# Kernel optimization log

Measured on AMD Instinct MI355X. Metric: run time of the kernel, lower is better.

Reference implementation:

```python
import jax, jax.numpy as jnp
import numpy as np

H_GRU = 32  # GRU hidden size fixed to 32 in the module


def setup_inputs() -> dict:
    key = jax.random.key(0)
    ks = jax.random.split(key, 12)
    B, C_in, H, W = 64, 64, 48, 160
    C_out = 64
    s_in = 1.0 / np.sqrt(C_in)
    s_h = 1.0 / np.sqrt(H_GRU)
    u = lambda k, shape: jax.random.uniform(k, shape, jnp.float32, -s_h, s_h)
    return {
        "x": jax.random.normal(ks[0], (B, C_in, H, W), jnp.float32),
        "conv_w": jax.random.normal(ks[1], (C_out, C_in), jnp.float32) * s_in,
        "conv_b": jax.random.normal(ks[2], (C_out,), jnp.float32) * s_in,
        "wih_f": u(ks[3], (3 * H_GRU, C_out)),
        "whh_f": u(ks[4], (3 * H_GRU, H_GRU)),
        "bih_f": u(ks[5], (3 * H_GRU,)),
        "bhh_f": u(ks[6], (3 * H_GRU,)),
        "wih_b": u(ks[7], (3 * H_GRU, C_out)),
        "whh_b": u(ks[8], (3 * H_GRU, H_GRU)),
        "bih_b": u(ks[9], (3 * H_GRU,)),
        "bhh_b": u(ks[10], (3 * H_GRU,)),
    }


def _gru_scan(pre, whh, bhh):
    # pre: [N, T, 3H] input-side gate pre-activations (already x@Wih^T + bih)
    N = pre.shape[0]

    def step(h, g):
        gh = h @ whh.T + bhh
        gi_r, gi_z, gi_n = jnp.split(g, 3, axis=-1)
        gh_r, gh_z, gh_n = jnp.split(gh, 3, axis=-1)
        r = jax.nn.sigmoid(gi_r + gh_r)
        z = jax.nn.sigmoid(gi_z + gh_z)
        n = jnp.tanh(gi_n + r * gh_n)
        h_new = (1.0 - z) * n + z * h
        return h_new, h_new

    h0 = jnp.zeros((N, H_GRU), pre.dtype)
    _, ys = jax.lax.scan(step, h0, jnp.swapaxes(pre, 0, 1))  # ys: [T, N, H]
    return jnp.swapaxes(ys, 0, 1)  # [N, T, H]


def reference(x, conv_w, conv_b, wih_f, whh_f, bih_f, bhh_f,
              wih_b, whh_b, bih_b, bhh_b):
    B, C_in, H, W = x.shape
    # 1x1 conv fused with the NCHW->NHWC permute
    y = jnp.einsum('bchw,oc->bhwo', x, conv_w) + conv_b  # [B, H, W, C_out]
    C_out = y.shape[-1]
    seq = y.reshape(B * H, W, C_out)  # GRU batch = B*H, seq_len = W
    # forward direction
    pre_f = jnp.einsum('ntc,gc->ntg', seq, wih_f) + bih_f
    out_f = _gru_scan(pre_f, whh_f, bhh_f)
    # backward direction: scan reversed sequence, then flip output back
    seq_r = seq[:, ::-1, :]
    pre_b = jnp.einsum('ntc,gc->ntg', seq_r, wih_b) + bih_b
    out_b = _gru_scan(pre_b, whh_b, bhh_b)[:, ::-1, :]
    out = jnp.concatenate([out_f, out_b], axis=-1)  # [B*H, W, 2*H_GRU]
    out = out.reshape(B, H, W, 2 * H_GRU)
    return jnp.transpose(out, (0, 3, 1, 2))  # back to NCHW
```

## Files before the change

### kernel.cpp

```cpp
#include <hip/hip_runtime.h>


typedef _Float16 f16x8 __attribute__((ext_vector_type(8)));
typedef _Float16 f16x4 __attribute__((ext_vector_type(4)));
typedef __fp16   pk16  __attribute__((ext_vector_type(2)));
typedef float    f32x4 __attribute__((ext_vector_type(4)));

#define HWSTRIDE 7680
#define WS_WHH2_OFF 24576
#define WS_BIAS_OFF 36864
#define WS_X16_OFF  65536
#define NWIN 20

__global__ void fold_weights(const float* __restrict__ conv_w,
                             const float* __restrict__ conv_b,
                             const float* __restrict__ wih_f,
                             const float* __restrict__ bih_f,
                             const float* __restrict__ bhh_f,
                             const float* __restrict__ wih_b,
                             const float* __restrict__ bih_b,
                             const float* __restrict__ bhh_b,
                             const float* __restrict__ whh_f,
                             const float* __restrict__ whh_b,
                             void* wsv)
{
    _Float16* W2   = (_Float16*)wsv;
    _Float16* whh2 = (_Float16*)((char*)wsv + WS_WHH2_OFF);
    float*    bias = (float*)((char*)wsv + WS_BIAS_OFF);
    const int idx = blockIdx.x * 256 + threadIdx.x;
    if (idx < 12288) {
        const int d = idx / 6144, r = idx % 6144, g = r / 64, c = r % 64;
        const float* wih = d ? wih_b : wih_f;
        float acc = 0.f;
        for (int o = 0; o < 64; ++o) acc += wih[g * 64 + o] * conv_w[o * 64 + c];
        W2[idx] = (_Float16)acc;
    } else if (idx < 18432) {
        const int e2 = idx - 12288;
        const int dd = e2 / 3072, rr = e2 % 3072, g = rr / 32, k = rr % 32;
        const int qq = k >> 3, ee = k & 7;
        const int jsrc = (ee < 4) ? (qq * 4 + ee) : (16 + qq * 4 + (ee - 4));
        const float* whh = dd ? whh_b : whh_f;
        whh2[e2] = (_Float16)whh[g * 32 + jsrc];
    } else if (idx < 18688) {
        const int e = idx - 18432;
        const int d = e >> 7, rr = e & 127, kind = rr >> 5, j = rr & 31;
        const float* wih = d ? wih_b : wih_f;
        const float* bih = d ? bih_b : bih_f;
        const float* bhh = d ? bhh_b : bhh_f;
        float v;
        if (kind == 0 || kind == 1) {
            const int g = j + kind * 32;
            float b2 = bih[g];
            for (int o = 0; o < 64; ++o) b2 += wih[g * 64 + o] * conv_b[o];
            v = b2 + bhh[g];
        } else if (kind == 2) {
            const int g = j + 64;
            float b2 = bih[g];
            for (int o = 0; o < 64; ++o) b2 += wih[g * 64 + o] * conv_b[o];
            v = b2;
        } else {
            v = bhh[j + 64];
        }
        bias[(d * 4 + kind) * 32 + j] = v;
    }
}

static __device__ __forceinline__ unsigned pkh(float a, float b) {
    pk16 p = __builtin_amdgcn_cvt_pkrtz(a, b);
    return __builtin_bit_cast(unsigned, p);
}

__global__ __launch_bounds__(256, 2)
void xpose(const float* __restrict__ x, _Float16* __restrict__ x16)
{
    __shared__ _Float16 tile[16 * 16 * 64];
    const int bid = blockIdx.x;
    const int wc  = bid % 10;
    const int hg  = (bid / 10) % 3;
    const int b   = bid / 30;
    const int t   = threadIdx.x;
    const int s   = t >> 4;
    const int c2  = t & 15;
    const float* xb = x + (size_t)b * 64 * HWSTRIDE + (size_t)(hg * 16) * 160 + wc * 16;

    float4 pf[4][4];
    #pragma unroll
    for (int cc = 0; cc < 4; ++cc)
        #pragma unroll
        for (int k = 0; k < 4; ++k)
            pf[cc][k] = *(const float4*)(xb + (size_t)(c2 * 4 + cc) * HWSTRIDE
                                         + (size_t)s * 160 + k * 4);
    #pragma unroll
    for (int k = 0; k < 4; ++k)
        #pragma unroll
        for (int m = 0; m < 4; ++m) {
            const int w = k * 4 + m;
            uint2 v;
            v.x = pkh(((const float*)&pf[0][k])[m], ((const float*)&pf[1][k])[m]);
            v.y = pkh(((const float*)&pf[2][k])[m], ((const float*)&pf[3][k])[m]);
            const int baddr = (s * 2048 + w * 128 + c2 * 8) ^ ((s & 7) << 4);
            *(uint2*)((char*)tile + baddr) = v;
        }
    __syncthreads();
    #pragma unroll
    for (int k = 0; k < 4; ++k) {
        const int w  = k * 4 + (t >> 6);
        const int ss = (t & 63) >> 2;
        const int c0 = (t & 3) * 16;
        uint2 dv[4];
        #pragma unroll
        for (int j = 0; j < 4; ++j) {
            const int baddr = (ss * 2048 + w * 128 + c0 * 2 + j * 8) ^ ((ss & 7) << 4);
            dv[j] = *(const uint2*)((char*)tile + baddr);
        }
        _Float16* op = x16 + ((size_t)(b * 3 + hg) * 160 + wc * 16 + w) * 1024 + ss * 64 + c0;
        *(uint4*)(op)     = make_uint4(dv[0].x, dv[0].y, dv[1].x, dv[1].y);
        *(uint4*)(op + 8) = make_uint4(dv[2].x, dv[2].y, dv[3].x, dv[3].y);
    }
}

__global__ __launch_bounds__(64, 1)
void gru_fused9(const _Float16* __restrict__ x16,
                const void* __restrict__ wsv,
                float* __restrict__ out)
{
    const int bid   = blockIdx.x;
    const int d     = bid & 1;
    const int slice = bid >> 1;
    const int b     = slice / 3;
    const int hg    = slice % 3;
    const int h0    = hg * 16;
    const int lane  = threadIdx.x;
    const int q     = lane >> 4;
    const int s16   = lane & 15;

    const _Float16* W2 = (const _Float16*)wsv + (size_t)d * 96 * 64;
    f16x8 W2A[6][2];
    #pragma unroll
    for (int gt = 0; gt < 6; ++gt)
        #pragma unroll
        for (int kt = 0; kt < 2; ++kt)
            W2A[gt][kt] = *(const f16x8*)&W2[(gt * 16 + s16) * 64 + kt * 32 + q * 8];
    const _Float16* whh2 = (const _Float16*)((const char*)wsv + WS_WHH2_OFF)
                           + (size_t)d * 96 * 32;
    f16x8 whhA[6];
    #pragma unroll
    for (int gt = 0; gt < 6; ++gt)
        whhA[gt] = *(const f16x8*)&whh2[(gt * 16 + s16) * 32 + q * 8];
    const float* bias = (const float*)((const char*)wsv + WS_BIAS_OFF) + d * 128;
    float biasC[6][4];
    #pragma unroll
    for (int gt = 0; gt < 6; ++gt)
        #pragma unroll
        for (int r = 0; r < 4; ++r)
            biasC[gt][r] = bias[(gt >> 1) * 32 + (gt & 1) * 16 + 4 * q + r];
    float bhN[2][4];
    #pragma unroll
    for (int jh = 0; jh < 2; ++jh)
        #pragma unroll
        for (int r = 0; r < 4; ++r)
            bhN[jh][r] = bias[96 + jh * 16 + 4 * q + r];

    const _Float16* xsl = x16 + (size_t)slice * 160 * 1024 + s16 * 64 + q * 8;
    float* ob = out + ((size_t)b * 64 + d * 32) * HWSTRIDE + (size_t)(h0 + s16) * 160;

    f16x8 B0r[4], B1r[4];
    auto loadB = [&](int s, f16x8& B0d, f16x8& B1d) {
        const _Float16* p = xsl + (size_t)(d ? (159 - s) : s) * 1024;
        B0d = *(const f16x8*)(p);
        B1d = *(const f16x8*)(p + 32);
    };
    #pragma unroll
    for (int s0 = 0; s0 < 4; ++s0) loadB(s0, B0r[s0], B1r[s0]);

    f16x8 hB = {};
    f16x8 hB8[8];
    float hprev[8];
    #pragma unroll
    for (int uu = 0; uu < 8; ++uu) hprev[uu] = 0.f;

    #pragma unroll 1
    for (int i = 0; i < NWIN; ++i) {
        #pragma unroll
        for (int tt = 0; tt < 8; ++tt) {
            const int s = i * 8 + tt;
            f32x4 aR0 = {biasC[0][0], biasC[0][1], biasC[0][2], biasC[0][3]};
            f32x4 aR1 = {biasC[1][0], biasC[1][1], biasC[1][2], biasC[1][3]};
            f32x4 aZ0 = {biasC[2][0], biasC[2][1], biasC[2][2], biasC[2][3]};
            f32x4 aZ1 = {biasC[3][0], biasC[3][1], biasC[3][2], biasC[3][3]};
            f32x4 pN0 = {biasC[4][0], biasC[4][1], biasC[4][2], biasC[4][3]};
            f32x4 pN1 = {biasC[5][0], biasC[5][1], biasC[5][2], biasC[5][3]};
            f32x4 hN0 = {bhN[0][0], bhN[0][1], bhN[0][2], bhN[0][3]};
            f32x4 hN1 = {bhN[1][0], bhN[1][1], bhN[1][2], bhN[1][3]};
            aR0 = __builtin_amdgcn_mfma_f32_16x16x32_f16(W2A[0][0], B0r[tt & 3], aR0, 0, 0, 0);
            aR0 = __builtin_amdgcn_mfma_f32_16x16x32_f16(W2A[0][1], B1r[tt & 3], aR0, 0, 0, 0);
            aR1 = __builtin_amdgcn_mfma_f32_16x16x32_f16(W2A[1][0], B0r[tt & 3], aR1, 0, 0, 0);
            aR1 = __builtin_amdgcn_mfma_f32_16x16x32_f16(W2A[1][1], B1r[tt & 3], aR1, 0, 0, 0);
            aZ0 = __builtin_amdgcn_mfma_f32_16x16x32_f16(W2A[2][0], B0r[tt & 3], aZ0, 0, 0, 0);
            aZ0 = __builtin_amdgcn_mfma_f32_16x16x32_f16(W2A[2][1], B1r[tt & 3], aZ0, 0, 0, 0);
            aZ1 = __builtin_amdgcn_mfma_f32_16x16x32_f16(W2A[3][0], B0r[tt & 3], aZ1, 0, 0, 0);
            aZ1 = __builtin_amdgcn_mfma_f32_16x16x32_f16(W2A[3][1], B1r[tt & 3], aZ1, 0, 0, 0);
            pN0 = __builtin_amdgcn_mfma_f32_16x16x32_f16(W2A[4][0], B0r[tt & 3], pN0, 0, 0, 0);
            pN0 = __builtin_amdgcn_mfma_f32_16x16x32_f16(W2A[4][1], B1r[tt & 3], pN0, 0, 0, 0);
            pN1 = __builtin_amdgcn_mfma_f32_16x16x32_f16(W2A[5][0], B0r[tt & 3], pN1, 0, 0, 0);
            pN1 = __builtin_amdgcn_mfma_f32_16x16x32_f16(W2A[5][1], B1r[tt & 3], pN1, 0, 0, 0);
            aR0 = __builtin_amdgcn_mfma_f32_16x16x32_f16(whhA[0], hB, aR0, 0, 0, 0);
            aR1 = __builtin_amdgcn_mfma_f32_16x16x32_f16(whhA[1], hB, aR1, 0, 0, 0);
            aZ0 = __builtin_amdgcn_mfma_f32_16x16x32_f16(whhA[2], hB, aZ0, 0, 0, 0);
            aZ1 = __builtin_amdgcn_mfma_f32_16x16x32_f16(whhA[3], hB, aZ1, 0, 0, 0);
            hN0 = __builtin_amdgcn_mfma_f32_16x16x32_f16(whhA[4], hB, hN0, 0, 0, 0);
            hN1 = __builtin_amdgcn_mfma_f32_16x16x32_f16(whhA[5], hB, hN1, 0, 0, 0);
            if (tt < 4) {
                loadB(s + 4, B0r[tt & 3], B1r[tt & 3]);
            } else if (i + 1 < NWIN) {
                loadB(s + 4, B0r[tt & 3], B1r[tt & 3]);
            }
            float hn[8];
            #pragma unroll
            for (int r = 0; r < 4; ++r) {
                const float rr = __builtin_amdgcn_rcpf(1.f + __expf(-aR0[r]));
                const float zz = __builtin_amdgcn_rcpf(1.f + __expf(-aZ0[r]));
                float ta = fmaf(rr, hN0[r], pN0[r]);
                ta = fminf(fmaxf(ta, -15.f), 15.f);
                const float e2 = __expf(2.f * ta);
                const float nn = (e2 - 1.f) * __builtin_amdgcn_rcpf(e2 + 1.f);
                hn[r] = (1.f - zz) * nn + zz * hprev[r];
            }
            #pragma unroll
            for (int r = 0; r < 4; ++r) {
                const float rr = __builtin_amdgcn_rcpf(1.f + __expf(-aR1[r]));
                const float zz = __builtin_amdgcn_rcpf(1.f + __expf(-aZ1[r]));
                float ta = fmaf(rr, hN1[r], pN1[r]);
                ta = fminf(fmaxf(ta, -15.f), 15.f);
                const float e2 = __expf(2.f * ta);
                const float nn = (e2 - 1.f) * __builtin_amdgcn_rcpf(e2 + 1.f);
                hn[4 + r] = (1.f - zz) * nn + zz * hprev[4 + r];
            }
            {
                uint4 hu;
                hu.x = pkh(hn[0], hn[1]); hu.y = pkh(hn[2], hn[3]);
                hu.z = pkh(hn[4], hn[5]); hu.w = pkh(hn[6], hn[7]);
                hB = __builtin_bit_cast(f16x8, hu);
            }
            hB8[tt] = hB;
            #pragma unroll
            for (int uu = 0; uu < 8; ++uu) hprev[uu] = hn[uu];
        }
        {
            const int w0 = d ? (152 - 8 * i) : (8 * i);
            #pragma unroll
            for (int e = 0; e < 8; ++e) {
                const int j = (e >> 2) * 16 + 4 * q + (e & 3);
                float* pw = ob + (size_t)j * HWSTRIDE + w0;
                if (d == 0) {
                    *(float4*)(pw)     = make_float4((float)hB8[0][e], (float)hB8[1][e],
                                                     (float)hB8[2][e], (float)hB8[3][e]);
                    *(float4*)(pw + 4) = make_float4((float)hB8[4][e], (float)hB8[5][e],
                                                     (float)hB8[6][e], (float)hB8[7][e]);
                } else {
                    *(float4*)(pw)     = make_float4((float)hB8[7][e], (float)hB8[6][e],
                                                     (float)hB8[5][e], (float)hB8[4][e]);
                    *(float4*)(pw + 4) = make_float4((float)hB8[3][e], (float)hB8[2][e],
                                                     (float)hB8[1][e], (float)hB8[0][e]);
                }
            }
        }
    }
}

#define BAR() do { asm volatile("s_waitcnt lgkmcnt(0)" ::: "memory"); \
                   __builtin_amdgcn_s_barrier();                      \
                   asm volatile("" ::: "memory"); } while (0)

__global__ __launch_bounds__(128, 1)
void gru_fused8(const float* __restrict__ x,
                const void* __restrict__ wsv,
                float* __restrict__ out)
{
    __shared__ __align__(16) _Float16 xt[1024 * 8];
    __shared__ __align__(16) _Float16 spre[2 * 8 * 16 * 96];

    const int bid  = blockIdx.x;
    const int d    = bid / 192;
    const int g    = bid % 192;
    const int b    = g / 3;
    const int h0   = (g % 3) * 16;
    const int lane = threadIdx.x & 63;
    const int wave = threadIdx.x >> 6;
    const int sw   = bid & 1;
    const int q    = lane >> 4;
    const int s16  = lane & 15;

    const float* xb = x + (size_t)b * 64 * HWSTRIDE + (size_t)h0 * 160;

    if (wave != sw) {
        const _Float16* W2 = (const _Float16*)wsv + (size_t)d * 96 * 64;
        f16x8 W2A[6][2];
        #pragma unroll
        for (int gt = 0; gt < 6; ++gt)
            #pragma unroll
            for (int kt = 0; kt < 2; ++kt)
                W2A[gt][kt] = *(const f16x8*)&W2[(gt * 16 + s16) * 64 + kt * 32 + q * 8];
        const float* bias = (const float*)((const char*)wsv + WS_BIAS_OFF) + d * 128;
        float biasC[6][4];
        #pragma unroll
        for (int gt = 0; gt < 6; ++gt)
            #pragma unroll
            for (int r = 0; r < 4; ++r)
                biasC[gt][r] = bias[(gt >> 1) * 32 + (gt & 1) * 16 + 4 * q + r];

        float4 pf[32];
        auto load_win = [&](int wi) {
            const int w0 = d ? (152 - 8 * wi) : (8 * wi);
            #pragma unroll
            for (int k = 0; k < 16; ++k) {
                const int row = lane + 64 * k;
                const float* p = xb + (size_t)(row >> 4) * HWSTRIDE + (row & 15) * 160 + w0;
                pf[2 * k]     = *(const float4*)p;
                pf[2 * k + 1] = *(const float4*)(p + 4);
            }
        };
        auto write_xt = [&]() {
            #pragma unroll
            for (int k = 0; k < 16; ++k) {
                const int row = lane + 64 * k;
                uint4 v;
                v.x = pkh(pf[2*k].x,   pf[2*k].y);
                v.y = pkh(pf[2*k].z,   pf[2*k].w);
                v.z = pkh(pf[2*k+1].x, pf[2*k+1].y);
                v.w = pkh(pf[2*k+1].z, pf[2*k+1].w);
                *(uint4*)&xt[row * 8] = v;
            }
        };
        auto project = [&](int wi) {
            _Float16* sp = &spre[(wi & 1) * 12288];
            for (int tt = 0; tt < 8; ++tt) {
                const int wl = d ? (7 - tt) : tt;
                const int base0 = (q * 8) * 128 + s16 * 8 + wl;
                f16x8 B0, B1;
                #pragma unroll
                for (int e = 0; e < 8; ++e) {
                    B0[e] = xt[base0 + e * 128];
                    B1[e] = xt[base0 + e * 128 + 4096];
                }
                #pragma unroll
                for (int gt = 0; gt < 6; ++gt) {
                    f32x4 acc = {biasC[gt][0], biasC[gt][1], biasC[gt][2], biasC[gt][3]};
                    acc = __builtin_amdgcn_mfma_f32_16x16x32_f16(W2A[gt][0], B0, acc, 0, 0, 0);
                    acc = __builtin_amdgcn_mfma_f32_16x16x32_f16(W2A[gt][1], B1, acc, 0, 0, 0);
                    uint2 v; v.x = pkh(acc[0], acc[1]); v.y = pkh(acc[2], acc[3]);
                    const int col = (gt * 16 + 4 * q) ^ ((s16 & 7) << 2);
                    *(uint2*)&sp[(tt * 16 + s16) * 96 + col] = v;
                }
            }
        };

        load_win(0);
        #pragma unroll 1
        for (int i = 0; i < NWIN; ++i) {
            write_xt();
            project(i);
            if (i + 1 < NWIN) load_win(i + 1);
            BAR();
        }
    } else {
        const _Float16* whh2 = (const _Float16*)((const char*)wsv + WS_WHH2_OFF)
                               + (size_t)d * 96 * 32;
        f16x8 whhA[6];
        #pragma unroll
        for (int gt = 0; gt < 6; ++gt)
            whhA[gt] = *(const f16x8*)&whh2[(gt * 16 + s16) * 32 + q * 8];
        const float* bias = (const float*)((const char*)wsv + WS_BIAS_OFF) + d * 128;
        float bhN[2][4];
        #pragma unroll
        for (int jh = 0; jh < 2; ++jh)
            #pragma unroll
            for (int r = 0; r < 4; ++r)
                bhN[jh][r] = bias[96 + jh * 16 + 4 * q + r];

        float* ob = out + ((size_t)b * 64 + d * 32) * HWSTRIDE + (size_t)(h0 + s16) * 160;
        f16x8 hB = {};
        f16x8 hB8[8];
        float hprev[8];
        #pragma unroll
        for (int uu = 0; uu < 8; ++uu) hprev[uu] = 0.f;

        int spcol[6];
        #pragma unroll
        for (int gt = 0; gt < 6; ++gt)
            spcol[gt] = (gt * 16 + 4 * q) ^ ((s16 & 7) << 2);

        #pragma unroll 1
        for (int i = 0; i < NWIN; ++i) {
            BAR();
            const _Float16* sp = &spre[(i & 1) * 12288];
            f16x4 pg[4][6];
            #pragma unroll
            for (int tt = 0; tt < 8; ++tt) {
                if ((tt & 3) == 0) {
                    #pragma unroll
                    for (int t4 = 0; t4 < 4; ++t4)
                        #pragma unroll
                        for (int gt = 0; gt < 6; ++gt)
                            pg[t4][gt] = *(const f16x4*)
                                &sp[((tt + t4) * 16 + s16) * 96 + spcol[gt]];
                }
                const f16x4 p0 = pg[tt & 3][0], p1 = pg[tt & 3][1];
                const f16x4 p2 = pg[tt & 3][2], p3 = pg[tt & 3][3];
                const f16x4 p4 = pg[tt & 3][4], p5 = pg[tt & 3][5];
                f32x4 aR0 = {(float)p0[0], (float)p0[1], (float)p0[2], (float)p0[3]};
                f32x4 aR1 = {(float)p1[0], (float)p1[1], (float)p1[2], (float)p1[3]};
                f32x4 aZ0 = {(float)p2[0], (float)p2[1], (float)p2[2], (float)p2[3]};
                f32x4 aZ1 = {(float)p3[0], (float)p3[1], (float)p3[2], (float)p3[3]};
                f32x4 aN0 = {bhN[0][0], bhN[0][1], bhN[0][2], bhN[0][3]};
                f32x4 aN1 = {bhN[1][0], bhN[1][1], bhN[1][2], bhN[1][3]};
                aR0 = __builtin_amdgcn_mfma_f32_16x16x32_f16(whhA[0], hB, aR0, 0, 0, 0);
                aR1 = __builtin_amdgcn_mfma_f32_16x16x32_f16(whhA[1], hB, aR1, 0, 0, 0);
                aZ0 = __builtin_amdgcn_mfma_f32_16x16x32_f16(whhA[2], hB, aZ0, 0, 0, 0);
                aZ1 = __builtin_amdgcn_mfma_f32_16x16x32_f16(whhA[3], hB, aZ1, 0, 0, 0);
                aN0 = __builtin_amdgcn_mfma_f32_16x16x32_f16(whhA[4], hB, aN0, 0, 0, 0);
                aN1 = __builtin_amdgcn_mfma_f32_16x16x32_f16(whhA[5], hB, aN1, 0, 0, 0);
                float hn[8];
                #pragma unroll
                for (int r = 0; r < 4; ++r) {
                    const float rr = __builtin_amdgcn_rcpf(1.f + __expf(-aR0[r]));
                    const float zz = __builtin_amdgcn_rcpf(1.f + __expf(-aZ0[r]));
                    float ta = fmaf(rr, aN0[r], (float)p4[r]);
                    ta = fminf(fmaxf(ta, -15.f), 15.f);
                    const float e2 = __expf(2.f * ta);
                    const float nn = (e2 - 1.f) * __builtin_amdgcn_rcpf(e2 + 1.f);
                    hn[r] = (1.f - zz) * nn + zz * hprev[r];
                }
                #pragma unroll
                for (int r = 0; r < 4; ++r) {
                    const float rr = __builtin_amdgcn_rcpf(1.f + __expf(-aR1[r]));
                    const float zz = __builtin_amdgcn_rcpf(1.f + __expf(-aZ1[r]));
                    float ta = fmaf(rr, aN1[r], (float)p5[r]);
                    ta = fminf(fmaxf(ta, -15.f), 15.f);
                    const float e2 = __expf(2.f * ta);
                    const float nn = (e2 - 1.f) * __builtin_amdgcn_rcpf(e2 + 1.f);
                    hn[4 + r] = (1.f - zz) * nn + zz * hprev[4 + r];
                }
                {
                    uint4 hu;
                    hu.x = pkh(hn[0], hn[1]); hu.y = pkh(hn[2], hn[3]);
                    hu.z = pkh(hn[4], hn[5]); hu.w = pkh(hn[6], hn[7]);
                    hB = __builtin_bit_cast(f16x8, hu);
                }
                hB8[tt] = hB;
                #pragma unroll
                for (int uu = 0; uu < 8; ++uu) hprev[uu] = hn[uu];
            }
            {
                const int w0 = d ? (152 - 8 * i) : (8 * i);
                #pragma unroll
                for (int e = 0; e < 8; ++e) {
                    const int j = (e >> 2) * 16 + 4 * q + (e & 3);
                    float* pw = ob + (size_t)j * HWSTRIDE + w0;
                    if (d == 0) {
                        *(float4*)(pw) = make_float4((float)hB8[0][e], (float)hB8[1][e],
                                                     (float)hB8[2][e], (float)hB8[3][e]);
                        *(float4*)(pw + 4) = make_float4((float)hB8[4][e], (float)hB8[5][e],
                                                         (float)hB8[6][e], (float)hB8[7][e]);
                    } else {
                        *(float4*)(pw) = make_float4((float)hB8[7][e], (float)hB8[6][e],
                                                     (float)hB8[5][e], (float)hB8[4][e]);
                        *(float4*)(pw + 4) = make_float4((float)hB8[3][e], (float)hB8[2][e],
                                                         (float)hB8[1][e], (float)hB8[0][e]);
                    }
                }
            }
        }
    }
}

extern "C" void kernel_launch(void* const* d_in, const int* in_sizes, int n_in,
                              void* d_out, int out_size, void* d_ws, size_t ws_size,
                              hipStream_t stream) {
    (void)in_sizes; (void)n_in; (void)out_size;
    fold_weights<<<dim3(74), dim3(256), 0, stream>>>(
        (const float*)d_in[1],
        (const float*)d_in[2],
        (const float*)d_in[3],
        (const float*)d_in[5],
        (const float*)d_in[6],
        (const float*)d_in[7],
        (const float*)d_in[9],
        (const float*)d_in[10],
        (const float*)d_in[4],
        (const float*)d_in[8],
        d_ws);
    const size_t need = (size_t)WS_X16_OFF + (size_t)192 * 160 * 1024 * 2;
    if (ws_size >= need) {
        _Float16* x16 = (_Float16*)((char*)d_ws + WS_X16_OFF);
        xpose<<<dim3(1920), dim3(256), 0, stream>>>((const float*)d_in[0], x16);
        gru_fused9<<<dim3(384), dim3(64), 0, stream>>>(x16, d_ws, (float*)d_out);
    } else {
        gru_fused8<<<dim3(384), dim3(128), 0, stream>>>(
            (const float*)d_in[0], d_ws, (float*)d_out);
    }
}
```

Measured before the change: 204.6 us.

## Stage GRU input windows through LDS with async global_load_lds double buffering

The GRU kernel now copies 16-timestep windows of the fp16 input straight into double-buffered, swizzled shared memory with global_load_lds. The next window is staged while the current one is processed, and B operands are read from shared memory one step ahead, replacing the per-step register prefetch from global memory. Output stores are batched per 16 steps, giving four float4 writes per row. The xpose kernel splits its loads into two halves and raises its occupancy hint, trading some load-level parallelism for lower register pressure. The full vmcnt(0) wait at each window boundary may stall the recurrence.

```diff
diff --git a/kernel.cpp b/kernel.cpp
--- a/kernel.cpp
+++ b/kernel.cpp
@@ -2,7 +2,6 @@
 
 
 typedef _Float16 f16x8 __attribute__((ext_vector_type(8)));
-typedef _Float16 f16x4 __attribute__((ext_vector_type(4)));
 typedef __fp16   pk16  __attribute__((ext_vector_type(2)));
 typedef float    f32x4 __attribute__((ext_vector_type(4)));
 
@@ -10,7 +9,9 @@
 #define WS_WHH2_OFF 24576
 #define WS_BIAS_OFF 36864
 #define WS_X16_OFF  65536
-#define NWIN 20
+
+typedef __attribute__((address_space(1))) const unsigned asg_t;
+typedef __attribute__((address_space(3))) unsigned asl_t;
 
 __global__ void fold_weights(const float* __restrict__ conv_w,
                              const float* __restrict__ conv_b,
@@ -70,7 +71,7 @@
     return __builtin_bit_cast(unsigned, p);
 }
 
-__global__ __launch_bounds__(256, 2)
+__global__ __launch_bounds__(256, 4)
 void xpose(const float* __restrict__ x, _Float16* __restrict__ x16)
 {
     __shared__ _Float16 tile[16 * 16 * 64];
@@ -83,24 +84,27 @@
     const int c2  = t & 15;
     const float* xb = x + (size_t)b * 64 * HWSTRIDE + (size_t)(hg * 16) * 160 + wc * 16;
 
-    float4 pf[4][4];
-    #pragma unroll
-    for (int cc = 0; cc < 4; ++cc)
-        #pragma unroll
-        for (int k = 0; k < 4; ++k)
-            pf[cc][k] = *(const float4*)(xb + (size_t)(c2 * 4 + cc) * HWSTRIDE
-                                         + (size_t)s * 160 + k * 4);
-    #pragma unroll
-    for (int k = 0; k < 4; ++k)
-        #pragma unroll
-        for (int m = 0; m < 4; ++m) {
-            const int w = k * 4 + m;
-            uint2 v;
-            v.x = pkh(((const float*)&pf[0][k])[m], ((const float*)&pf[1][k])[m]);
-            v.y = pkh(((const float*)&pf[2][k])[m], ((const float*)&pf[3][k])[m]);
-            const int baddr = (s * 2048 + w * 128 + c2 * 8) ^ ((s & 7) << 4);
-            *(uint2*)((char*)tile + baddr) = v;
-        }
+    #pragma unroll
+    for (int half = 0; half < 2; ++half) {
+        float4 pf[4][2];
+        #pragma unroll
+        for (int cc = 0; cc < 4; ++cc)
+            #pragma unroll
+            for (int k = 0; k < 2; ++k)
+                pf[cc][k] = *(const float4*)(xb + (size_t)(c2 * 4 + cc) * HWSTRIDE
+                                             + (size_t)s * 160 + (half * 2 + k) * 4);
+        #pragma unroll
+        for (int k = 0; k < 2; ++k)
+            #pragma unroll
+            for (int m = 0; m < 4; ++m) {
+                const int w = (half * 2 + k) * 4 + m;
+                uint2 v;
+                v.x = pkh(((const float*)&pf[0][k])[m], ((const float*)&pf[1][k])[m]);
+                v.y = pkh(((const float*)&pf[2][k])[m], ((const float*)&pf[3][k])[m]);
+                const int baddr = (s * 2048 + w * 128 + c2 * 8) ^ ((s & 7) << 4);
+                *(uint2*)((char*)tile + baddr) = v;
+            }
+    }
     __syncthreads();
     #pragma unroll
     for (int k = 0; k < 4; ++k) {
@@ -120,16 +124,17 @@
 }
 
 __global__ __launch_bounds__(64, 1)
-void gru_fused9(const _Float16* __restrict__ x16,
-                const void* __restrict__ wsv,
-                float* __restrict__ out)
+void gru_fused12(const _Float16* __restrict__ x16,
+                 const void* __restrict__ wsv,
+                 float* __restrict__ out)
 {
+    __shared__ __align__(16) _Float16 wb[2][16][1024];
+
     const int bid   = blockIdx.x;
     const int d     = bid & 1;
     const int slice = bid >> 1;
     const int b     = slice / 3;
-    const int hg    = slice % 3;
-    const int h0    = hg * 16;
+    const int h0    = (slice % 3) * 16;
     const int lane  = threadIdx.x;
     const int q     = lane >> 4;
     const int s16   = lane & 15;
@@ -161,29 +166,51 @@
         for (int r = 0; r < 4; ++r)
             bhN[jh][r] = bias[96 + jh * 16 + 4 * q + r];
 
-    const _Float16* xsl = x16 + (size_t)slice * 160 * 1024 + s16 * 64 + q * 8;
     float* ob = out + ((size_t)b * 64 + d * 32) * HWSTRIDE + (size_t)(h0 + s16) * 160;
 
-    f16x8 B0r[4], B1r[4];
-    auto loadB = [&](int s, f16x8& B0d, f16x8& B1d) {
-        const _Float16* p = xsl + (size_t)(d ? (159 - s) : s) * 1024;
-        B0d = *(const f16x8*)(p);
-        B1d = *(const f16x8*)(p + 32);
+    const int tq  = (lane ^ (lane >> 3)) & 7;
+    const size_t go0 = (size_t)((lane >> 3) * 128 + (tq >> 2) * 64 + (tq & 3) * 16);
+    const size_t go1 = go0 + 1024;
+    const char* xg = (const char*)(x16 + (size_t)slice * 160 * 1024);
+
+    auto stage = [&](int wi, int pb) {
+        #pragma unroll
+        for (int tt = 0; tt < 16; ++tt) {
+            const int sg = d ? (159 - (wi * 16 + tt)) : (wi * 16 + tt);
+            const char* gp = xg + (size_t)sg * 2048;
+            __builtin_amdgcn_global_load_lds((asg_t*)(gp + go0),
+                                             (asl_t*)&wb[pb][tt][0],   16, 0, 0);
+            __builtin_amdgcn_global_load_lds((asg_t*)(gp + go1),
+                                             (asl_t*)&wb[pb][tt][512], 16, 0, 0);
+        }
     };
-    #pragma unroll
-    for (int s0 = 0; s0 < 4; ++s0) loadB(s0, B0r[s0], B1r[s0]);
+
+    const int rb0o = (s16 * 128 + q * 16)      ^ ((s16 & 7) << 4);
+    const int rb1o = (s16 * 128 + q * 16 + 64) ^ ((s16 & 7) << 4);
+    auto rdB = [&](int pb, int tt, f16x8& B0, f16x8& B1) {
+        const char* base = (const char*)&wb[pb][tt][0];
+        B0 = *(const f16x8*)(base + rb0o);
+        B1 = *(const f16x8*)(base + rb1o);
+    };
+
+    stage(0, 0);
+    asm volatile("s_waitcnt vmcnt(0)" ::: "memory");
+    f16x8 B0c, B1c, B0n, B1n;
+    rdB(0, 0, B0c, B1c);
 
     f16x8 hB = {};
-    f16x8 hB8[8];
+    f16x8 hB16[16];
     float hprev[8];
     #pragma unroll
     for (int uu = 0; uu < 8; ++uu) hprev[uu] = 0.f;
 
     #pragma unroll 1
-    for (int i = 0; i < NWIN; ++i) {
-        #pragma unroll
-        for (int tt = 0; tt < 8; ++tt) {
-            const int s = i * 8 + tt;
+    for (int wi = 0; wi < 10; ++wi) {
+        const int pb = wi & 1;
+        if (wi + 1 < 10) stage(wi + 1, pb ^ 1);
+        #pragma unroll
+        for (int tt = 0; tt < 16; ++tt) {
+            if (tt < 15) rdB(pb, tt + 1, B0n, B1n);
             f32x4 aR0 = {biasC[0][0], biasC[0][1], biasC[0][2], biasC[0][3]};
             f32x4 aR1 = {biasC[1][0], biasC[1][1], biasC[1][2], biasC[1][3]};
             f32x4 aZ0 = {biasC[2][0], biasC[2][1], biasC[2][2], biasC[2][3]};
@@ -192,29 +219,24 @@
             f32x4 pN1 = {biasC[5][0], biasC[5][1], biasC[5][2], biasC[5][3]};
             f32x4 hN0 = {bhN[0][0], bhN[0][1], bhN[0][2], bhN[0][3]};
             f32x4 hN1 = {bhN[1][0], bhN[1][1], bhN[1][2], bhN[1][3]};
-            aR0 = __builtin_amdgcn_mfma_f32_16x16x32_f16(W2A[0][0], B0r[tt & 3], aR0, 0, 0, 0);
-            aR0 = __builtin_amdgcn_mfma_f32_16x16x32_f16(W2A[0][1], B1r[tt & 3], aR0, 0, 0, 0);
-            aR1 = __builtin_amdgcn_mfma_f32_16x16x32_f16(W2A[1][0], B0r[tt & 3], aR1, 0, 0, 0);
-            aR1 = __builtin_amdgcn_mfma_f32_16x16x32_f16(W2A[1][1], B1r[tt & 3], aR1, 0, 0, 0);
-            aZ0 = __builtin_amdgcn_mfma_f32_16x16x32_f16(W2A[2][0], B0r[tt & 3], aZ0, 0, 0, 0);
-            aZ0 = __builtin_amdgcn_mfma_f32_16x16x32_f16(W2A[2][1], B1r[tt & 3], aZ0, 0, 0, 0);
-            aZ1 = __builtin_amdgcn_mfma_f32_16x16x32_f16(W2A[3][0], B0r[tt & 3], aZ1, 0, 0, 0);
-            aZ1 = __builtin_amdgcn_mfma_f32_16x16x32_f16(W2A[3][1], B1r[tt & 3], aZ1, 0, 0, 0);
-            pN0 = __builtin_amdgcn_mfma_f32_16x16x32_f16(W2A[4][0], B0r[tt & 3], pN0, 0, 0, 0);
-            pN0 = __builtin_amdgcn_mfma_f32_16x16x32_f16(W2A[4][1], B1r[tt & 3], pN0, 0, 0, 0);
-            pN1 = __builtin_amdgcn_mfma_f32_16x16x32_f16(W2A[5][0], B0r[tt & 3], pN1, 0, 0, 0);
-            pN1 = __builtin_amdgcn_mfma_f32_16x16x32_f16(W2A[5][1], B1r[tt & 3], pN1, 0, 0, 0);
+            aR0 = __builtin_amdgcn_mfma_f32_16x16x32_f16(W2A[0][0], B0c, aR0, 0, 0, 0);
+            aR0 = __builtin_amdgcn_mfma_f32_16x16x32_f16(W2A[0][1], B1c, aR0, 0, 0, 0);
+            aR1 = __builtin_amdgcn_mfma_f32_16x16x32_f16(W2A[1][0], B0c, aR1, 0, 0, 0);
+            aR1 = __builtin_amdgcn_mfma_f32_16x16x32_f16(W2A[1][1], B1c, aR1, 0, 0, 0);
+            aZ0 = __builtin_amdgcn_mfma_f32_16x16x32_f16(W2A[2][0], B0c, aZ0, 0, 0, 0);
+            aZ0 = __builtin_amdgcn_mfma_f32_16x16x32_f16(W2A[2][1], B1c, aZ0, 0, 0, 0);
+            aZ1 = __builtin_amdgcn_mfma_f32_16x16x32_f16(W2A[3][0], B0c, aZ1, 0, 0, 0);
+            aZ1 = __builtin_amdgcn_mfma_f32_16x16x32_f16(W2A[3][1], B1c, aZ1, 0, 0, 0);
+            pN0 = __builtin_amdgcn_mfma_f32_16x16x32_f16(W2A[4][0], B0c, pN0, 0, 0, 0);
+            pN0 = __builtin_amdgcn_mfma_f32_16x16x32_f16(W2A[4][1], B1c, pN0, 0, 0, 0);
+            pN1 = __builtin_amdgcn_mfma_f32_16x16x32_f16(W2A[5][0], B0c, pN1, 0, 0, 0);
+            pN1 = __builtin_amdgcn_mfma_f32_16x16x32_f16(W2A[5][1], B1c, pN1, 0, 0, 0);
             aR0 = __builtin_amdgcn_mfma_f32_16x16x32_f16(whhA[0], hB, aR0, 0, 0, 0);
             aR1 = __builtin_amdgcn_mfma_f32_16x16x32_f16(whhA[1], hB, aR1, 0, 0, 0);
             aZ0 = __builtin_amdgcn_mfma_f32_16x16x32_f16(whhA[2], hB, aZ0, 0, 0, 0);
             aZ1 = __builtin_amdgcn_mfma_f32_16x16x32_f16(whhA[3], hB, aZ1, 0, 0, 0);
             hN0 = __builtin_amdgcn_mfma_f32_16x16x32_f16(whhA[4], hB, hN0, 0, 0, 0);
             hN1 = __builtin_amdgcn_mfma_f32_16x16x32_f16(whhA[5], hB, hN1, 0, 0, 0);
-            if (tt < 4) {
-                loadB(s + 4, B0r[tt & 3], B1r[tt & 3]);
-            } else if (i + 1 < NWIN) {
-                loadB(s + 4, B0r[tt & 3], B1r[tt & 3]);
-            }
             float hn[8];
             #pragma unroll
             for (int r = 0; r < 4; ++r) {
@@ -242,35 +264,40 @@
                 hu.z = pkh(hn[4], hn[5]); hu.w = pkh(hn[6], hn[7]);
                 hB = __builtin_bit_cast(f16x8, hu);
             }
-            hB8[tt] = hB;
+            hB16[tt] = hB;
             #pragma unroll
             for (int uu = 0; uu < 8; ++uu) hprev[uu] = hn[uu];
+            B0c = B0n; B1c = B1n;
+        }
+        if (wi + 1 < 10) {
+            asm volatile("s_waitcnt vmcnt(0)" ::: "memory");
+            rdB(pb ^ 1, 0, B0c, B1c);
         }
         {
-            const int w0 = d ? (152 - 8 * i) : (8 * i);
+            const int w0 = d ? (144 - 16 * wi) : (16 * wi);
             #pragma unroll
             for (int e = 0; e < 8; ++e) {
-                const int j = (e >> 2) * 16 + 4 * q + (e & 3);
-                float* pw = ob + (size_t)j * HWSTRIDE + w0;
-                if (d == 0) {
-                    *(float4*)(pw)     = make_float4((float)hB8[0][e], (float)hB8[1][e],
-                                                     (float)hB8[2][e], (float)hB8[3][e]);
-                    *(float4*)(pw + 4) = make_float4((float)hB8[4][e], (float)hB8[5][e],
-                                                     (float)hB8[6][e], (float)hB8[7][e]);
-                } else {
-                    *(float4*)(pw)     = make_float4((float)hB8[7][e], (float)hB8[6][e],
-                                                     (float)hB8[5][e], (float)hB8[4][e]);
-                    *(float4*)(pw + 4) = make_float4((float)hB8[3][e], (float)hB8[2][e],
-                                                     (float)hB8[1][e], (float)hB8[0][e]);
+                const int jj = (e >> 2) * 16 + 4 * q + (e & 3);
+                float* pw = ob + (size_t)jj * HWSTRIDE + w0;
+                #pragma unroll
+                for (int m = 0; m < 4; ++m) {
+                    float4 v;
+                    if (d == 0)
+                        v = make_float4((float)hB16[4*m][e],   (float)hB16[4*m+1][e],
+                                        (float)hB16[4*m+2][e], (float)hB16[4*m+3][e]);
+                    else
+                        v = make_float4((float)hB16[15-4*m][e], (float)hB16[14-4*m][e],
+                                        (float)hB16[13-4*m][e], (float)hB16[12-4*m][e]);
+                    *(float4*)(pw + 4 * m) = v;
                 }
             }
         }
     }
 }
 
-#define BAR() do { asm volatile("s_waitcnt lgkmcnt(0)" ::: "memory"); \
-                   __builtin_amdgcn_s_barrier();                      \
-                   asm volatile("" ::: "memory"); } while (0)
+#define BARX() do { asm volatile("s_waitcnt lgkmcnt(0)" ::: "memory"); \
+                    __builtin_amdgcn_s_barrier();                      \
+                    asm volatile("" ::: "memory"); } while (0)
 
 __global__ __launch_bounds__(128, 1)
 void gru_fused8(const float* __restrict__ x,
@@ -357,11 +384,11 @@
 
         load_win(0);
         #pragma unroll 1
-        for (int i = 0; i < NWIN; ++i) {
+        for (int i = 0; i < 20; ++i) {
             write_xt();
             project(i);
-            if (i + 1 < NWIN) load_win(i + 1);
-            BAR();
+            if (i + 1 < 20) load_win(i + 1);
+            BARX();
         }
     } else {
         const _Float16* whh2 = (const _Float16*)((const char*)wsv + WS_WHH2_OFF)
@@ -390,11 +417,12 @@
         for (int gt = 0; gt < 6; ++gt)
             spcol[gt] = (gt * 16 + 4 * q) ^ ((s16 & 7) << 2);
 
+        typedef _Float16 f16x4l __attribute__((ext_vector_type(4)));
         #pragma unroll 1
-        for (int i = 0; i < NWIN; ++i) {
-            BAR();
+        for (int i = 0; i < 20; ++i) {
+            BARX();
             const _Float16* sp = &spre[(i & 1) * 12288];
-            f16x4 pg[4][6];
+            f16x4l pg[4][6];
             #pragma unroll
             for (int tt = 0; tt < 8; ++tt) {
                 if ((tt & 3) == 0) {
@@ -402,12 +430,12 @@
                     for (int t4 = 0; t4 < 4; ++t4)
                         #pragma unroll
                         for (int gt = 0; gt < 6; ++gt)
-                            pg[t4][gt] = *(const f16x4*)
+                            pg[t4][gt] = *(const f16x4l*)
                                 &sp[((tt + t4) * 16 + s16) * 96 + spcol[gt]];
                 }
-                const f16x4 p0 = pg[tt & 3][0], p1 = pg[tt & 3][1];
-                const f16x4 p2 = pg[tt & 3][2], p3 = pg[tt & 3][3];
-                const f16x4 p4 = pg[tt & 3][4], p5 = pg[tt & 3][5];
+                const f16x4l p0 = pg[tt & 3][0], p1 = pg[tt & 3][1];
+                const f16x4l p2 = pg[tt & 3][2], p3 = pg[tt & 3][3];
+                const f16x4l p4 = pg[tt & 3][4], p5 = pg[tt & 3][5];
                 f32x4 aR0 = {(float)p0[0], (float)p0[1], (float)p0[2], (float)p0[3]};
                 f32x4 aR1 = {(float)p1[0], (float)p1[1], (float)p1[2], (float)p1[3]};
                 f32x4 aZ0 = {(float)p2[0], (float)p2[1], (float)p2[2], (float)p2[3]};
@@ -494,7 +522,7 @@
     if (ws_size >= need) {
         _Float16* x16 = (_Float16*)((char*)d_ws + WS_X16_OFF);
         xpose<<<dim3(1920), dim3(256), 0, stream>>>((const float*)d_in[0], x16);
-        gru_fused9<<<dim3(384), dim3(64), 0, stream>>>(x16, d_ws, (float*)d_out);
+        gru_fused12<<<dim3(384), dim3(64), 0, stream>>>(x16, d_ws, (float*)d_out);
     } else {
         gru_fused8<<<dim3(384), dim3(128), 0, stream>>>(
             (const float*)d_in[0], d_ws, (float*)d_out);
```

New measurement: 206.4 us. About the same (+0.9%).
